# Performance work log

Hardware: AMD Instinct MI355X
Metric: run time of the kernel (lower is better)

Reference implementation:

```python
import jax, jax.numpy as jnp
import numpy as np

B, T, C = 4, 2048, 1024
H = 16
DH = C // H  # 64


def setup_inputs() -> dict:
    key = jax.random.key(0)
    ks = jax.random.split(key, 10)
    s_in = 1.0 / np.sqrt(C)
    x = jax.random.normal(ks[0], (B, T, C), dtype=jnp.float32)
    # stacked per-head projection weights: [H, C, DH]
    Wq = jax.random.normal(ks[1], (H, C, DH), dtype=jnp.float32) * s_in
    bq = jnp.zeros((H, DH), dtype=jnp.float32)
    Wk = jax.random.normal(ks[2], (H, C, DH), dtype=jnp.float32) * s_in
    bk = jnp.zeros((H, DH), dtype=jnp.float32)
    Wv = jax.random.normal(ks[3], (H, C, DH), dtype=jnp.float32) * s_in
    bv = jnp.zeros((H, DH), dtype=jnp.float32)
    Wo = jax.random.normal(ks[4], (C, C), dtype=jnp.float32) * s_in
    bo = jnp.zeros((C,), dtype=jnp.float32)
    return {"x": x, "Wq": Wq, "bq": bq, "Wk": Wk, "bk": bk,
            "Wv": Wv, "bv": bv, "Wo": Wo, "bo": bo}


def reference(x, Wq, bq, Wk, bk, Wv, bv, Wo, bo):
    # per-head projections: (B,T,C) x (H,C,DH) -> (B,H,T,DH)
    q = jnp.einsum('btc,hcd->bhtd', x, Wq) + bq[None, :, None, :]
    k = jnp.einsum('btc,hcd->bhtd', x, Wk) + bk[None, :, None, :]
    v = jnp.einsum('btc,hcd->bhtd', x, Wv) + bv[None, :, None, :]
    # scores scaled by C**-0.5 (C = full input embedding dim, as in source)
    scale = jnp.float32(C) ** -0.5
    scores = jnp.einsum('bhtd,bhsd->bhts', q, k) * scale  # (B,H,T,T)
    causal = jnp.tril(jnp.ones((T, T), dtype=bool))
    scores = jnp.where(causal, scores, -jnp.inf)
    attn = jax.nn.softmax(scores, axis=-1)
    out = jnp.einsum('bhts,bhsd->bhtd', attn, v)  # (B,H,T,DH)
    out = out.transpose(0, 2, 1, 3).reshape(B, T, C)  # concat heads
    return out @ Wo + bo
```

## Files before the change

### kernel.cpp

```cpp
#include <hip/hip_runtime.h>
#include <hip/hip_bf16.h>

#define TDIM 2048
#define BDIM 4
#define CDIM 1024
#define HDIM 16
#define DH   64

typedef __hip_bfloat16 bf16;
typedef __attribute__((ext_vector_type(8))) short bf16x8;
typedef __attribute__((ext_vector_type(4))) short bf16x4;
typedef __attribute__((ext_vector_type(4))) float f32x4;

__device__ __forceinline__ void async_ld16(const bf16* g, bf16* l) {
    __builtin_amdgcn_global_load_lds(
        (const __attribute__((address_space(1))) unsigned int*)g,
        (__attribute__((address_space(3))) unsigned int*)l, 16, 0, 0);
}

__device__ __forceinline__ unsigned short bf16bits(float x) {
    bf16 b = __float2bfloat16(x);
    return *(unsigned short*)&b;
}

__device__ __forceinline__ f32x4 mfma_16x16x16_bf16(bf16x4 a, bf16x4 b, f32x4 c) {
#if __has_builtin(__builtin_amdgcn_mfma_f32_16x16x16_bf16)
    return __builtin_amdgcn_mfma_f32_16x16x16_bf16(a, b, c, 0, 0, 0);
#elif __has_builtin(__builtin_amdgcn_mfma_f32_16x16x16bf16_1k)
    return __builtin_amdgcn_mfma_f32_16x16x16bf16_1k(a, b, c, 0, 0, 0);
#else
    asm volatile("v_mfma_f32_16x16x16_bf16 %0, %1, %2, %0"
                 : "+v"(c) : "v"(a), "v"(b));
    return c;
#endif
}

__global__ void convert_x4(const float4* __restrict__ src, ushort4* __restrict__ dst, int n4) {
    int i = blockIdx.x * blockDim.x + threadIdx.x;
    if (i >= n4) return;
    float4 v = src[i];
    ushort4 o;
    o.x = bf16bits(v.x); o.y = bf16bits(v.y);
    o.z = bf16bits(v.z); o.w = bf16bits(v.w);
    dst[i] = o;
}

__global__ void convert_biases(const float* __restrict__ b0, const float* __restrict__ b1,
                               const float* __restrict__ b2, const float* __restrict__ b3,
                               bf16* __restrict__ dst) {
    int i = blockIdx.x * blockDim.x + threadIdx.x;
    int which = i >> 10, j = i & 1023;
    const float* src = (which == 0) ? b0 : (which == 1) ? b1 : (which == 2) ? b2 : b3;
    dst[i] = __float2bfloat16(src[j]);
}

__global__ __launch_bounds__(256) void transpose_qkv_kernel(
    const float* __restrict__ Wq, const float* __restrict__ Wk, const float* __restrict__ Wv,
    bf16* __restrict__ WqT, bf16* __restrict__ WkT, bf16* __restrict__ WvT) {
    __shared__ float tile[64][65];
    const int which = blockIdx.z >> 4, h = blockIdx.z & 15;
    const float* W  = ((which == 0) ? Wq  : (which == 1) ? Wk  : Wv)  + (size_t)h * CDIM * DH;
    bf16*        WT = ((which == 0) ? WqT : (which == 1) ? WkT : WvT) + (size_t)h * CDIM * DH;
    const int c0 = blockIdx.x * 64;
    for (int it = 0; it < 16; it++) {
        int e = it * 256 + threadIdx.x;
        int r = e >> 6, col = e & 63;
        tile[r][col] = W[(size_t)(c0 + r) * DH + col];
    }
    __syncthreads();
    for (int it = 0; it < 16; it++) {
        int e = it * 256 + threadIdx.x;
        int r = e >> 6, col = e & 63;
        WT[(size_t)r * CDIM + c0 + col] = __float2bfloat16(tile[col][r]);
    }
}

__global__ __launch_bounds__(256) void transpose_wo_kernel(
    const float* __restrict__ W, bf16* __restrict__ WT) {
    __shared__ float tile[64][65];
    const int c0 = blockIdx.x * 64, d0 = blockIdx.y * 64;
    for (int it = 0; it < 16; it++) {
        int e = it * 256 + threadIdx.x;
        int r = e >> 6, col = e & 63;
        tile[r][col] = W[(size_t)(c0 + r) * CDIM + d0 + col];
    }
    __syncthreads();
    for (int it = 0; it < 16; it++) {
        int e = it * 256 + threadIdx.x;
        int r = e >> 6, col = e & 63;
        WT[(size_t)(d0 + r) * CDIM + c0 + col] = __float2bfloat16(tile[col][r]);
    }
}

__global__ __launch_bounds__(256) void transpose_v_kernel(
    const bf16* __restrict__ V, bf16* __restrict__ Vt) {
    __shared__ unsigned short tile[64][65];
    const int bh = blockIdx.y, t0 = blockIdx.x * 64;
    const unsigned short* Vp  = (const unsigned short*)V + ((size_t)bh * TDIM + t0) * DH;
    unsigned short*       Vtp = (unsigned short*)Vt + (size_t)bh * DH * TDIM;
    for (int it = 0; it < 16; it++) {
        int e = it * 256 + threadIdx.x;
        int r = e >> 6, c = e & 63;
        tile[r][c] = Vp[(size_t)r * DH + c];
    }
    __syncthreads();
    for (int it = 0; it < 16; it++) {
        int e = it * 256 + threadIdx.x;
        int r = e >> 6, c = e & 63;
        Vtp[(size_t)r * TDIM + t0 + c] = tile[c][r];
    }
}

__global__ __launch_bounds__(256) void proj_qkv_kernel(
    const bf16* __restrict__ X,
    const bf16* __restrict__ WqT, const bf16* __restrict__ WkT, const bf16* __restrict__ WvT,
    const bf16* __restrict__ bq,  const bf16* __restrict__ bk,  const bf16* __restrict__ bvv,
    bf16* __restrict__ Qo, bf16* __restrict__ Ko, bf16* __restrict__ Vo)
{
    const int z = blockIdx.z;
    const bf16* Bt   = (z == 0) ? WqT : (z == 1) ? WkT : WvT;
    const bf16* bias = (z == 0) ? bq  : (z == 1) ? bk  : bvv;

    __shared__ __align__(16) bf16 As[128 * 32];
    __shared__ __align__(16) bf16 Bs[128 * 32];

    const int tid  = threadIdx.x;
    const int lane = tid & 63;
    const int wave = tid >> 6;
    const int wr = wave >> 1, wc = wave & 1;
    const int l15 = lane & 15, quad = lane >> 4;

    const int blockM = blockIdx.y * 128;
    const int blockN = blockIdx.x * 128;

    f32x4 acc[4][4];
    for (int i = 0; i < 4; i++)
        for (int j = 0; j < 4; j++)
            acc[i][j] = (f32x4){0.f, 0.f, 0.f, 0.f};

    const int srow = lane >> 2, scol = (lane & 3) * 8;
    for (int k0 = 0; k0 < CDIM; k0 += 32) {
        for (int cc = 0; cc < 2; cc++) {
            int chunk = wave * 2 + cc;
            int row = chunk * 16 + srow;
            async_ld16(&X [(size_t)(blockM + row) * CDIM + k0 + scol], &As[chunk * 512]);
            async_ld16(&Bt[(size_t)(blockN + row) * CDIM + k0 + scol], &Bs[chunk * 512]);
        }
        __syncthreads();

        bf16x8 af[4], bfr[4];
        for (int mi = 0; mi < 4; mi++)
            af[mi] = *(const bf16x8*)&As[(wr * 64 + mi * 16 + l15) * 32 + quad * 8];
        for (int ni = 0; ni < 4; ni++)
            bfr[ni] = *(const bf16x8*)&Bs[(wc * 64 + ni * 16 + l15) * 32 + quad * 8];

        for (int mi = 0; mi < 4; mi++)
            for (int ni = 0; ni < 4; ni++)
                acc[mi][ni] = __builtin_amdgcn_mfma_f32_16x16x32_bf16(
                    af[mi], bfr[ni], acc[mi][ni], 0, 0, 0);
        __syncthreads();
    }

    for (int mi = 0; mi < 4; mi++) {
        int mbase = blockM + wr * 64 + mi * 16 + quad * 4;
        for (int ni = 0; ni < 4; ni++) {
            int n = blockN + wc * 64 + ni * 16 + l15;
            float bval = __bfloat162float(bias[n]);
            int h = n >> 6, d = n & 63;
            for (int r = 0; r < 4; r++) {
                int mm = mbase + r;
                int b = mm >> 11, t = mm & 2047;
                float val = acc[mi][ni][r] + bval;
                size_t idx = (((size_t)b * HDIM + h) * TDIM + t) * DH + d;
                if (z == 0)      Qo[idx] = __float2bfloat16(val * 0.03125f);
                else if (z == 1) Ko[idx] = __float2bfloat16(val);
                else             Vo[idx] = __float2bfloat16(val);
            }
        }
    }
}

__global__ __launch_bounds__(256) void proj_out_kernel(
    const bf16* __restrict__ X, const bf16* __restrict__ Bt,
    const bf16* __restrict__ bias, float* __restrict__ Out)
{
    __shared__ __align__(16) bf16 As[128 * 32];
    __shared__ __align__(16) bf16 Bs[128 * 32];

    const int tid  = threadIdx.x;
    const int lane = tid & 63;
    const int wave = tid >> 6;
    const int wr = wave >> 1, wc = wave & 1;
    const int l15 = lane & 15, quad = lane >> 4;

    const int blockM = blockIdx.y * 128;
    const int blockN = blockIdx.x * 128;

    f32x4 acc[4][4];
    for (int i = 0; i < 4; i++)
        for (int j = 0; j < 4; j++)
            acc[i][j] = (f32x4){0.f, 0.f, 0.f, 0.f};

    const int srow = lane >> 2, scol = (lane & 3) * 8;
    for (int k0 = 0; k0 < CDIM; k0 += 32) {
        for (int cc = 0; cc < 2; cc++) {
            int chunk = wave * 2 + cc;
            int row = chunk * 16 + srow;
            async_ld16(&X [(size_t)(blockM + row) * CDIM + k0 + scol], &As[chunk * 512]);
            async_ld16(&Bt[(size_t)(blockN + row) * CDIM + k0 + scol], &Bs[chunk * 512]);
        }
        __syncthreads();

        bf16x8 af[4], bfr[4];
        for (int mi = 0; mi < 4; mi++)
            af[mi] = *(const bf16x8*)&As[(wr * 64 + mi * 16 + l15) * 32 + quad * 8];
        for (int ni = 0; ni < 4; ni++)
            bfr[ni] = *(const bf16x8*)&Bs[(wc * 64 + ni * 16 + l15) * 32 + quad * 8];

        for (int mi = 0; mi < 4; mi++)
            for (int ni = 0; ni < 4; ni++)
                acc[mi][ni] = __builtin_amdgcn_mfma_f32_16x16x32_bf16(
                    af[mi], bfr[ni], acc[mi][ni], 0, 0, 0);
        __syncthreads();
    }

    for (int mi = 0; mi < 4; mi++) {
        int mbase = blockM + wr * 64 + mi * 16 + quad * 4;
        for (int ni = 0; ni < 4; ni++) {
            int n = blockN + wc * 64 + ni * 16 + l15;
            float bval = __bfloat162float(bias[n]);
            for (int r = 0; r < 4; r++)
                Out[(size_t)(mbase + r) * CDIM + n] = acc[mi][ni][r] + bval;
        }
    }
}

__global__ __launch_bounds__(256) void attn_kernel(
    const bf16* __restrict__ Q, const bf16* __restrict__ Kb,
    const bf16* __restrict__ Vt, bf16* __restrict__ Y)
{
    const int bh    = blockIdx.y;
    const int qTile = (int)gridDim.x - 1 - blockIdx.x;
    const int qBase = qTile * 64;
    const int tid  = threadIdx.x;
    const int lane = tid & 63, wave = tid >> 6;
    const int l15 = lane & 15, quad = lane >> 4;

    __shared__ __align__(16) char smem[2 * 64 * 72 * 2 + 4 * 64 * 4];
    bf16*  Ks   = (bf16*)smem;
    bf16*  Vs   = Ks + 64 * 72;
    float* Of   = (float*)smem;
    float* dbuf = (float*)(smem + 2 * 64 * 72 * 2);

    bf16x8 qf[4][2];
    for (int nt = 0; nt < 4; nt++) {
        const size_t qrow = (size_t)bh * TDIM + qBase + nt * 16 + l15;
        qf[nt][0] = *(const bf16x8*)&Q[qrow * DH + quad * 8];
        qf[nt][1] = *(const bf16x8*)&Q[qrow * DH + 32 + quad * 8];
    }

    f32x4 o[4][4];
    for (int i = 0; i < 4; i++)
        for (int j = 0; j < 4; j++)
            o[i][j] = (f32x4){0.f, 0.f, 0.f, 0.f};
    float lsum[4] = {0.f, 0.f, 0.f, 0.f};

    const int r0 = tid >> 3, kc0 = (tid & 7) * 8;

    const int nkt = qTile + 1;
    uint4 kreg0 = *(const uint4*)&Kb[((size_t)bh * TDIM + r0) * DH + kc0];
    uint4 kreg1 = *(const uint4*)&Kb[((size_t)bh * TDIM + r0 + 32) * DH + kc0];
    uint4 vreg0 = *(const uint4*)&Vt[((size_t)bh * DH + r0) * TDIM + kc0];
    uint4 vreg1 = *(const uint4*)&Vt[((size_t)bh * DH + r0 + 32) * TDIM + kc0];

    for (int kt = 0; kt < nkt; kt++) {
        *(uint4*)&Ks[r0 * 72 + kc0]        = kreg0;
        *(uint4*)&Ks[(r0 + 32) * 72 + kc0] = kreg1;
        *(uint4*)&Vs[r0 * 72 + kc0]        = vreg0;
        *(uint4*)&Vs[(r0 + 32) * 72 + kc0] = vreg1;
        __syncthreads();

        if (kt + 1 < nkt) {
            const int nb = (kt + 1) * 64;
            kreg0 = *(const uint4*)&Kb[((size_t)bh * TDIM + nb + r0) * DH + kc0];
            kreg1 = *(const uint4*)&Kb[((size_t)bh * TDIM + nb + r0 + 32) * DH + kc0];
            vreg0 = *(const uint4*)&Vt[((size_t)bh * DH + r0) * TDIM + nb + kc0];
            vreg1 = *(const uint4*)&Vt[((size_t)bh * DH + r0 + 32) * TDIM + nb + kc0];
        }

        bf16x8 k0 = *(const bf16x8*)&Ks[(wave * 16 + l15) * 72 + quad * 8];
        bf16x8 k1 = *(const bf16x8*)&Ks[(wave * 16 + l15) * 72 + 32 + quad * 8];
        bf16x4 vA[4];
        for (int mt = 0; mt < 4; mt++)
            vA[mt] = *(const bf16x4*)&Vs[(mt * 16 + l15) * 72 + wave * 16 + quad * 4];

        f32x4 s[4];
        for (int nt = 0; nt < 4; nt++) {
            f32x4 a = (f32x4){0.f, 0.f, 0.f, 0.f};
            a = __builtin_amdgcn_mfma_f32_16x16x32_bf16(k0, qf[nt][0], a, 0, 0, 0);
            a = __builtin_amdgcn_mfma_f32_16x16x32_bf16(k1, qf[nt][1], a, 0, 0, 0);
            s[nt] = a;
        }

        const bool diag = (kt == qTile);
        const int keyg = kt * 64 + wave * 16 + quad * 4;
        for (int nt = 0; nt < 4; nt++) {
            const int qg = qBase + nt * 16 + l15;
            bf16x4 pb;
            for (int r = 0; r < 4; r++) {
                float pe = __expf(s[nt][r]);
                if (diag && (keyg + r > qg)) pe = 0.f;
                lsum[nt] += pe;
                pb[r] = (short)bf16bits(pe);
            }
            for (int mt = 0; mt < 4; mt++)
                o[mt][nt] = mfma_16x16x16_bf16(vA[mt], pb, o[mt][nt]);
        }
        __syncthreads();
    }

    float dsum[4];
    for (int nt = 0; nt < 4; nt++) {
        float v = lsum[nt];
        v += __shfl_xor(v, 16, 64);
        v += __shfl_xor(v, 32, 64);
        dsum[nt] = v;
    }
    if (quad == 0)
        for (int nt = 0; nt < 4; nt++)
            dbuf[wave * 64 + nt * 16 + l15] = dsum[nt];

    for (int w = 0; w < 4; w++) {
        if (wave == w) {
            for (int mt = 0; mt < 4; mt++)
                for (int nt = 0; nt < 4; nt++)
                    for (int r = 0; r < 4; r++) {
                        int d = mt * 16 + quad * 4 + r, q = nt * 16 + l15;
                        if (w == 0) Of[d * 68 + q]  = o[mt][nt][r];
                        else        Of[d * 68 + q] += o[mt][nt][r];
                    }
        }
        __syncthreads();
    }

    const int b = bh >> 4, h = bh & 15;
    const int q = tid >> 2, dc = (tid & 3) * 16;
    const float inv = 1.0f / (dbuf[q] + dbuf[64 + q] + dbuf[128 + q] + dbuf[192 + q]);
    for (int c = 0; c < 2; c++) {
        unsigned short pk[8];
        for (int j = 0; j < 8; j++)
            pk[j] = bf16bits(Of[(dc + c * 8 + j) * 68 + q] * inv);
        *(uint4*)&Y[((size_t)b * TDIM + qBase + q) * CDIM + h * DH + dc + c * 8] =
            *(uint4*)pk;
    }
}

extern "C" void kernel_launch(void* const* d_in, const int* in_sizes, int n_in,
                              void* d_out, int out_size, void* d_ws, size_t ws_size,
                              hipStream_t stream) {
    (void)in_sizes; (void)n_in; (void)out_size; (void)ws_size;

    char* ws = (char*)d_ws;
    const size_t SZ_BHTD = (size_t)BDIM * HDIM * TDIM * DH * sizeof(bf16);
    const size_t SZ_W    = (size_t)HDIM * CDIM * DH * sizeof(bf16);
    bf16* Qb  = (bf16*)(ws);
    bf16* Kb  = (bf16*)(ws + SZ_BHTD);
    bf16* Vt  = (bf16*)(ws + 2 * SZ_BHTD);
    bf16* Y   = (bf16*)(ws + 3 * SZ_BHTD);
    bf16* WqT = (bf16*)(ws + 4 * SZ_BHTD);
    bf16* WkT = (bf16*)(ws + 4 * SZ_BHTD + SZ_W);
    bf16* WvT = (bf16*)(ws + 4 * SZ_BHTD + 2 * SZ_W);
    bf16* WoT = (bf16*)(ws + 4 * SZ_BHTD + 3 * SZ_W);
    bf16* xC  = (bf16*)(ws + 4 * SZ_BHTD + 4 * SZ_W);
    bf16* bqC = (bf16*)(ws + 5 * SZ_BHTD + 4 * SZ_W);
    bf16* bkC = bqC + 1024;
    bf16* bvC = bqC + 2048;
    bf16* boC = bqC + 3072;
    bf16* Vb  = (bf16*)d_out;

    const int nX4 = (BDIM * TDIM * CDIM) / 4;
    convert_x4<<<nX4 / 256, 256, 0, stream>>>((const float4*)d_in[0], (ushort4*)xC, nX4);
    convert_biases<<<16, 256, 0, stream>>>((const float*)d_in[2], (const float*)d_in[4],
                                           (const float*)d_in[6], (const float*)d_in[8], bqC);

    transpose_qkv_kernel<<<dim3(CDIM / 64, 1, 48), 256, 0, stream>>>(
        (const float*)d_in[1], (const float*)d_in[3], (const float*)d_in[5], WqT, WkT, WvT);
    transpose_wo_kernel<<<dim3(CDIM / 64, CDIM / 64), 256, 0, stream>>>(
        (const float*)d_in[7], WoT);

    dim3 gq(CDIM / 128, (BDIM * TDIM) / 128, 3);
    proj_qkv_kernel<<<gq, 256, 0, stream>>>(xC, WqT, WkT, WvT, bqC, bkC, bvC, Qb, Kb, Vb);

    transpose_v_kernel<<<dim3(TDIM / 64, BDIM * HDIM), 256, 0, stream>>>(Vb, Vt);

    attn_kernel<<<dim3(TDIM / 64, BDIM * HDIM), 256, 0, stream>>>(Qb, Kb, Vt, Y);

    proj_out_kernel<<<dim3(CDIM / 128, (BDIM * TDIM) / 128), 256, 0, stream>>>(
        Y, WoT, boC, (float*)d_out);
}
```

Measured before the change: 328.9 us.

## Give each attention wave its own query rows with 128-query tiles

The attention kernel now processes 128 queries per block, and each wave owns 16 query rows in each of two 64-row groups. Previously each wave owned a slice of keys for all 64 queries. Each wave therefore iterates over every key chunk itself, which removes the cross-wave LDS reduction of partial outputs and row sums and its serialized barriers. Each K/V tile loaded into LDS is also reused across twice as many queries. In exchange each wave does more serial work per tile, the grid has half as many blocks, and the epilogue stages output through the Ks buffer after the final barrier.

After: 300.2 us. -8.7%, faster.

```diff
diff --git a/kernel.cpp b/kernel.cpp
--- a/kernel.cpp
+++ b/kernel.cpp
@@ -235,39 +235,36 @@
     }
 }
 
-__global__ __launch_bounds__(256) void attn_kernel(
+__global__ __launch_bounds__(256, 4) void attn_kernel(
     const bf16* __restrict__ Q, const bf16* __restrict__ Kb,
     const bf16* __restrict__ Vt, bf16* __restrict__ Y)
 {
     const int bh    = blockIdx.y;
-    const int qTile = (int)gridDim.x - 1 - blockIdx.x;
-    const int qBase = qTile * 64;
+    const int qT    = (int)gridDim.x - 1 - blockIdx.x;
+    const int qBase = qT * 128;
     const int tid  = threadIdx.x;
     const int lane = tid & 63, wave = tid >> 6;
     const int l15 = lane & 15, quad = lane >> 4;
 
-    __shared__ __align__(16) char smem[2 * 64 * 72 * 2 + 4 * 64 * 4];
-    bf16*  Ks   = (bf16*)smem;
-    bf16*  Vs   = Ks + 64 * 72;
-    float* Of   = (float*)smem;
-    float* dbuf = (float*)(smem + 2 * 64 * 72 * 2);
-
-    bf16x8 qf[4][2];
-    for (int nt = 0; nt < 4; nt++) {
-        const size_t qrow = (size_t)bh * TDIM + qBase + nt * 16 + l15;
-        qf[nt][0] = *(const bf16x8*)&Q[qrow * DH + quad * 8];
-        qf[nt][1] = *(const bf16x8*)&Q[qrow * DH + 32 + quad * 8];
-    }
-
-    f32x4 o[4][4];
-    for (int i = 0; i < 4; i++)
-        for (int j = 0; j < 4; j++)
-            o[i][j] = (f32x4){0.f, 0.f, 0.f, 0.f};
-    float lsum[4] = {0.f, 0.f, 0.f, 0.f};
+    __shared__ __align__(16) bf16 Ks[64 * 72];
+    __shared__ __align__(16) bf16 Vs[64 * 72];
+
+    bf16x8 qf[2][2];
+    for (int g = 0; g < 2; g++) {
+        const size_t qrow = (size_t)bh * TDIM + qBase + g * 64 + wave * 16 + l15;
+        qf[g][0] = *(const bf16x8*)&Q[qrow * DH + quad * 8];
+        qf[g][1] = *(const bf16x8*)&Q[qrow * DH + 32 + quad * 8];
+    }
+
+    f32x4 o[2][4];
+    for (int g = 0; g < 2; g++)
+        for (int mt = 0; mt < 4; mt++)
+            o[g][mt] = (f32x4){0.f, 0.f, 0.f, 0.f};
+    float lsum[2] = {0.f, 0.f};
 
     const int r0 = tid >> 3, kc0 = (tid & 7) * 8;
 
-    const int nkt = qTile + 1;
+    const int nkt = 2 * qT + 2;
     uint4 kreg0 = *(const uint4*)&Kb[((size_t)bh * TDIM + r0) * DH + kc0];
     uint4 kreg1 = *(const uint4*)&Kb[((size_t)bh * TDIM + r0 + 32) * DH + kc0];
     uint4 vreg0 = *(const uint4*)&Vt[((size_t)bh * DH + r0) * TDIM + kc0];
@@ -288,70 +285,53 @@
             vreg1 = *(const uint4*)&Vt[((size_t)bh * DH + r0 + 32) * TDIM + nb + kc0];
         }
 
-        bf16x8 k0 = *(const bf16x8*)&Ks[(wave * 16 + l15) * 72 + quad * 8];
-        bf16x8 k1 = *(const bf16x8*)&Ks[(wave * 16 + l15) * 72 + 32 + quad * 8];
-        bf16x4 vA[4];
-        for (int mt = 0; mt < 4; mt++)
-            vA[mt] = *(const bf16x4*)&Vs[(mt * 16 + l15) * 72 + wave * 16 + quad * 4];
-
-        f32x4 s[4];
+        const int dg = kt - 2 * qT;
         for (int nt = 0; nt < 4; nt++) {
-            f32x4 a = (f32x4){0.f, 0.f, 0.f, 0.f};
-            a = __builtin_amdgcn_mfma_f32_16x16x32_bf16(k0, qf[nt][0], a, 0, 0, 0);
-            a = __builtin_amdgcn_mfma_f32_16x16x32_bf16(k1, qf[nt][1], a, 0, 0, 0);
-            s[nt] = a;
-        }
-
-        const bool diag = (kt == qTile);
-        const int keyg = kt * 64 + wave * 16 + quad * 4;
-        for (int nt = 0; nt < 4; nt++) {
-            const int qg = qBase + nt * 16 + l15;
-            bf16x4 pb;
-            for (int r = 0; r < 4; r++) {
-                float pe = __expf(s[nt][r]);
-                if (diag && (keyg + r > qg)) pe = 0.f;
-                lsum[nt] += pe;
-                pb[r] = (short)bf16bits(pe);
+            bf16x8 kf0 = *(const bf16x8*)&Ks[(nt * 16 + l15) * 72 + quad * 8];
+            bf16x8 kf1 = *(const bf16x8*)&Ks[(nt * 16 + l15) * 72 + 32 + quad * 8];
+            bf16x4 vA[4];
+            for (int mt = 0; mt < 4; mt++)
+                vA[mt] = *(const bf16x4*)&Vs[(mt * 16 + l15) * 72 + nt * 16 + quad * 4];
+
+            for (int g = 0; g < 2; g++) {
+                if (dg == 1 && g == 0) continue;
+                f32x4 s = (f32x4){0.f, 0.f, 0.f, 0.f};
+                s = __builtin_amdgcn_mfma_f32_16x16x32_bf16(kf0, qf[g][0], s, 0, 0, 0);
+                s = __builtin_amdgcn_mfma_f32_16x16x32_bf16(kf1, qf[g][1], s, 0, 0, 0);
+
+                const bool diag = (dg == g);
+                bf16x4 pb;
+                for (int r = 0; r < 4; r++) {
+                    float pe = __expf(s[r]);
+                    if (diag && (nt * 16 + quad * 4 + r > wave * 16 + l15)) pe = 0.f;
+                    lsum[g] += pe;
+                    pb[r] = (short)bf16bits(pe);
+                }
+                for (int mt = 0; mt < 4; mt++)
+                    o[g][mt] = mfma_16x16x16_bf16(vA[mt], pb, o[g][mt]);
             }
-            for (int mt = 0; mt < 4; mt++)
-                o[mt][nt] = mfma_16x16x16_bf16(vA[mt], pb, o[mt][nt]);
-        }
-        __syncthreads();
-    }
-
-    float dsum[4];
-    for (int nt = 0; nt < 4; nt++) {
-        float v = lsum[nt];
+        }
+        __syncthreads();
+    }
+
+    const int b = bh >> 4, h = bh & 15;
+    for (int g = 0; g < 2; g++) {
+        float v = lsum[g];
         v += __shfl_xor(v, 16, 64);
         v += __shfl_xor(v, 32, 64);
-        dsum[nt] = v;
-    }
-    if (quad == 0)
-        for (int nt = 0; nt < 4; nt++)
-            dbuf[wave * 64 + nt * 16 + l15] = dsum[nt];
-
-    for (int w = 0; w < 4; w++) {
-        if (wave == w) {
-            for (int mt = 0; mt < 4; mt++)
-                for (int nt = 0; nt < 4; nt++)
-                    for (int r = 0; r < 4; r++) {
-                        int d = mt * 16 + quad * 4 + r, q = nt * 16 + l15;
-                        if (w == 0) Of[d * 68 + q]  = o[mt][nt][r];
-                        else        Of[d * 68 + q] += o[mt][nt][r];
-                    }
-        }
-        __syncthreads();
-    }
-
-    const int b = bh >> 4, h = bh & 15;
-    const int q = tid >> 2, dc = (tid & 3) * 16;
-    const float inv = 1.0f / (dbuf[q] + dbuf[64 + q] + dbuf[128 + q] + dbuf[192 + q]);
-    for (int c = 0; c < 2; c++) {
-        unsigned short pk[8];
-        for (int j = 0; j < 8; j++)
-            pk[j] = bf16bits(Of[(dc + c * 8 + j) * 68 + q] * inv);
-        *(uint4*)&Y[((size_t)b * TDIM + qBase + q) * CDIM + h * DH + dc + c * 8] =
-            *(uint4*)pk;
+        const float inv = 1.0f / v;
+
+        for (int mt = 0; mt < 4; mt++) {
+            unsigned short pk[4];
+            for (int r = 0; r < 4; r++) pk[r] = bf16bits(o[g][mt][r] * inv);
+            *(ushort4*)&Ks[(wave * 16 + l15) * 72 + mt * 16 + quad * 4] = *(ushort4*)pk;
+        }
+        const int qq = lane >> 2, part = lane & 3;
+        const int t = qBase + g * 64 + wave * 16 + qq;
+        uint4 c0 = *(const uint4*)&Ks[(wave * 16 + qq) * 72 + part * 16];
+        uint4 c1 = *(const uint4*)&Ks[(wave * 16 + qq) * 72 + part * 16 + 8];
+        *(uint4*)&Y[((size_t)b * TDIM + t) * CDIM + h * DH + part * 16]     = c0;
+        *(uint4*)&Y[((size_t)b * TDIM + t) * CDIM + h * DH + part * 16 + 8] = c1;
     }
 }
 
@@ -393,7 +373,7 @@
 
     transpose_v_kernel<<<dim3(TDIM / 64, BDIM * HDIM), 256, 0, stream>>>(Vb, Vt);
 
-    attn_kernel<<<dim3(TDIM / 64, BDIM * HDIM), 256, 0, stream>>>(Qb, Kb, Vt, Y);
+    attn_kernel<<<dim3(TDIM / 128, BDIM * HDIM), 256, 0, stream>>>(Qb, Kb, Vt, Y);
 
     proj_out_kernel<<<dim3(CDIM / 128, (BDIM * TDIM) / 128), 256, 0, stream>>>(
         Y, WoT, boC, (float*)d_out);
```
